# Performance work log

Hardware: AMD Instinct MI355X
Metric: run time of the kernel (lower is better)

## Reference

```python
import jax, jax.numpy as jnp
import numpy as np

N_HEADS = 16
PROJ_DIM = 64  # per-head dim
DIM = N_HEADS * PROJ_DIM  # 1024


def setup_inputs() -> dict:
    key = jax.random.key(0)
    k1, k2, k3, k4, k5 = jax.random.split(key, 5)
    N, L = 2, 2048
    scale = 1.0 / np.sqrt(DIM)
    return {
        "query": jax.random.normal(k1, (N, L, DIM), dtype=jnp.float32),
        "key": jax.random.normal(k2, (N, L, DIM), dtype=jnp.float32),
        "Wq": jax.random.normal(k3, (DIM, DIM), dtype=jnp.float32) * scale,
        "Wk": jax.random.normal(k4, (DIM, DIM), dtype=jnp.float32) * scale,
        "Wv": jax.random.normal(k5, (DIM, DIM), dtype=jnp.float32) * scale,
    }


def reference(query, key, Wq, Wk, Wv):
    # Causal linear-complexity attention (mask=True branch, left_first=False).
    N, Lq, _ = query.shape
    Lk = key.shape[1]
    H, Dh = N_HEADS, PROJ_DIM
    # torch Linear: x @ W.T ; reshape to (N, H, L, Dh)
    q = (query @ Wq.T).reshape(N, Lq, H, Dh).transpose(0, 2, 1, 3)
    k = (key @ Wk.T).reshape(N, Lk, H, Dh).transpose(0, 2, 1, 3)
    v = (key @ Wv.T).reshape(N, Lk, H, Dh).transpose(0, 2, 1, 3)
    q = jax.nn.softmax(q, axis=-1)
    k = jax.nn.softmax(k, axis=-1)
    # right[t] = sum_{s<=t} k_s^T v_s  : (N,H,Lk,Dh,Dh) cumulative outer products
    S = jnp.cumsum(jnp.einsum('nhti,nhtj->nhtij', k, v), axis=2)
    out = jnp.einsum('nhti,nhtij->nhtj', q, S)  # (N,H,Lq,Dh)
    return out.transpose(0, 2, 1, 3).reshape(N, Lq, H * Dh)
```

## Files before the change

kernel.cpp:

```cpp
#include <hip/hip_runtime.h>


constexpr int DIM  = 1024;
constexpr int H    = 16;
constexpr int DH   = 64;
constexpr int LSEQ = 2048;
constexpr int NB   = 2;
constexpr int MTOK = NB * LSEQ;
constexpr int CS   = 64;
constexpr int NC   = LSEQ / CS;

typedef __bf16 bf16x8 __attribute__((ext_vector_type(8)));
typedef float floatx4 __attribute__((ext_vector_type(4)));
typedef unsigned short ushort_t;

__device__ __forceinline__ ushort_t f2bf(float f) {
  unsigned int u = __float_as_uint(f);
  u += 0x7FFFu + ((u >> 16) & 1u);
  return (ushort_t)(u >> 16);
}
__device__ __forceinline__ float bf2f(ushort_t b) {
  return __uint_as_float(((unsigned int)b) << 16);
}

__device__ __forceinline__ void async16(void* lds, const void* g) {
  __builtin_amdgcn_global_load_lds(
      (const __attribute__((address_space(1))) unsigned int*)g,
      (__attribute__((address_space(3))) unsigned int*)lds, 16, 0, 0);
}

__device__ __forceinline__ bf16x8 tfrag(const unsigned int* T, int row, int uoff) {
  union { bf16x8 v; unsigned int u[4]; } r;
  const unsigned int* p = T + row * 33 + uoff;
  r.u[0] = p[0]; r.u[1] = p[1]; r.u[2] = p[2]; r.u[3] = p[3];
  return r.v;
}

__device__ __forceinline__ void transpose_tile(const ushort_t* g, unsigned int* TT, int tid) {
  const int ic = tid & 7, tp = tid >> 3;
  const ushort_t* r0 = g + (size_t)(2 * tp) * DIM + ic * 8;
  union { uint4 q; ushort_t u[8]; } a0, a1;
  a0.q = *(const uint4*)r0;
  a1.q = *(const uint4*)(r0 + DIM);
#pragma unroll
  for (int j = 0; j < 8; j++)
    TT[(8 * ic + j) * 33 + tp] = (unsigned int)a0.u[j] | ((unsigned int)a1.u[j] << 16);
}

__global__ __launch_bounds__(256) void cast_all(const float* __restrict__ q,
                                                const float* __restrict__ k,
                                                const float* __restrict__ wq,
                                                const float* __restrict__ wk,
                                                const float* __restrict__ wv,
                                                ushort_t* __restrict__ xbf,
                                                ushort_t* __restrict__ wbf) {
  const int seg = blockIdx.y;
  const float* src;
  ushort_t* dst;
  int n4;
  if (seg == 0)      { src = q;  dst = xbf;                  n4 = (4 << 20) / 4; }
  else if (seg == 1) { src = k;  dst = xbf + (4 << 20);      n4 = (4 << 20) / 4; }
  else if (seg == 2) { src = wq; dst = wbf;                  n4 = (1 << 20) / 4; }
  else if (seg == 3) { src = wk; dst = wbf + (1 << 20);      n4 = (1 << 20) / 4; }
  else               { src = wv; dst = wbf + (2 << 20);      n4 = (1 << 20) / 4; }
  for (int i = blockIdx.x * 256 + threadIdx.x; i < n4; i += gridDim.x * 256) {
    const float4 f = ((const float4*)src)[i];
    ((ushort4*)dst)[i] = make_ushort4(f2bf(f.x), f2bf(f.y), f2bf(f.z), f2bf(f.w));
  }
}

struct Stage { ushort_t As[128 * 32]; ushort_t Ws[128 * 32]; };
union SMemU { Stage st; ushort_t CsB[128 * 136]; };

__global__ __launch_bounds__(256) void gemm_fused(const ushort_t* __restrict__ xbf,
                                                  const ushort_t* __restrict__ wbf,
                                                  ushort_t* __restrict__ qp,
                                                  ushort_t* __restrict__ kp,
                                                  ushort_t* __restrict__ vp) {
  __shared__ SMemU sm;
  const int tid  = threadIdx.x;
  const int z    = blockIdx.z;
  const ushort_t* A = xbf + (z ? (size_t)(4 << 20) : 0);
  const ushort_t* W = wbf + (size_t)z * (1 << 20);
  ushort_t* C = (z == 0) ? qp : ((z == 1) ? kp : vp);
  const int bn   = blockIdx.x * 128;
  const int bm   = blockIdx.y * 128;
  const int lane = tid & 63;
  const int wid  = tid >> 6;
  const int wm   = wid >> 1, wn = wid & 1;
  const int row16 = lane & 15, quad = lane >> 4;

  floatx4 acc[4][4] = {};

  const ushort_t* gA0 = A + (size_t)(bm + (tid >> 2)) * DIM + (tid & 3) * 8;
  const ushort_t* gA1 = A + (size_t)(bm + 64 + (tid >> 2)) * DIM + (tid & 3) * 8;
  const ushort_t* gW0 = W + (size_t)(bn + (tid >> 2)) * DIM + (tid & 3) * 8;
  const ushort_t* gW1 = W + (size_t)(bn + 64 + (tid >> 2)) * DIM + (tid & 3) * 8;
  ushort_t* lA0 = sm.st.As + tid * 8;
  ushort_t* lA1 = sm.st.As + (tid + 256) * 8;
  ushort_t* lW0 = sm.st.Ws + tid * 8;
  ushort_t* lW1 = sm.st.Ws + (tid + 256) * 8;

  for (int k0 = 0; k0 < DIM; k0 += 32) {
    __syncthreads();
    async16(lA0, gA0 + k0);
    async16(lA1, gA1 + k0);
    async16(lW0, gW0 + k0);
    async16(lW1, gW1 + k0);
    __syncthreads();
    bf16x8 a[4], b[4];
#pragma unroll
    for (int mt = 0; mt < 4; mt++)
      a[mt] = *(const bf16x8*)&sm.st.As[(wm * 64 + mt * 16 + row16) * 32 + quad * 8];
#pragma unroll
    for (int nt = 0; nt < 4; nt++)
      b[nt] = *(const bf16x8*)&sm.st.Ws[(wn * 64 + nt * 16 + row16) * 32 + quad * 8];
#pragma unroll
    for (int mt = 0; mt < 4; mt++)
#pragma unroll
      for (int nt = 0; nt < 4; nt++)
        acc[mt][nt] = __builtin_amdgcn_mfma_f32_16x16x32_bf16(a[mt], b[nt], acc[mt][nt], 0, 0, 0);
  }
  __syncthreads();

  if (z < 2) {
#pragma unroll
    for (int mt = 0; mt < 4; mt++)
#pragma unroll
      for (int r = 0; r < 4; r++) {
        float m = fmaxf(fmaxf(acc[mt][0][r], acc[mt][1][r]),
                        fmaxf(acc[mt][2][r], acc[mt][3][r]));
#pragma unroll
        for (int o = 1; o < 16; o <<= 1) m = fmaxf(m, __shfl_xor(m, o, 64));
        float e[4], s = 0.f;
#pragma unroll
        for (int nt = 0; nt < 4; nt++) { e[nt] = __expf(acc[mt][nt][r] - m); s += e[nt]; }
#pragma unroll
        for (int o = 1; o < 16; o <<= 1) s += __shfl_xor(s, o, 64);
        const float inv = 1.f / s;
#pragma unroll
        for (int nt = 0; nt < 4; nt++) acc[mt][nt][r] = e[nt] * inv;
      }
  }

#pragma unroll
  for (int mt = 0; mt < 4; mt++)
#pragma unroll
    for (int nt = 0; nt < 4; nt++)
#pragma unroll
      for (int r = 0; r < 4; r++)
        sm.CsB[(wm * 64 + mt * 16 + quad * 4 + r) * 136 + wn * 64 + nt * 16 + row16] =
            f2bf(acc[mt][nt][r]);
  __syncthreads();
#pragma unroll
  for (int it = 0; it < 8; it++) {
    const int ch = tid + it * 256;
    const int row = ch >> 4, ic = ch & 15;
    const uint4 val = *(const uint4*)&sm.CsB[row * 136 + ic * 8];
    *(uint4*)&C[(size_t)(bm + row) * DIM + bn + ic * 8] = val;
  }
}

__global__ __launch_bounds__(256) void chunk_T(const ushort_t* __restrict__ kp,
                                               const ushort_t* __restrict__ vp,
                                               float* __restrict__ cs) {
  __shared__ unsigned int KT[64 * 33];
  __shared__ unsigned int VT[64 * 33];
  const int c = blockIdx.x, h = blockIdx.y, n = blockIdx.z;
  const int tid = threadIdx.x;
  const size_t gbase = ((size_t)(n * LSEQ + c * CS)) * DIM + h * DH;

  transpose_tile(kp + gbase, KT, tid);
  transpose_tile(vp + gbase, VT, tid);
  __syncthreads();

  const int lane = tid & 63, wid = tid >> 6;
  const int row16 = lane & 15, quad = lane >> 4;

  floatx4 acc[4] = {};
#pragma unroll
  for (int ks = 0; ks < 2; ks++) {
    const bf16x8 a = tfrag(VT, wid * 16 + row16, ks * 16 + quad * 4);
#pragma unroll
    for (int nt = 0; nt < 4; nt++) {
      const bf16x8 b = tfrag(KT, nt * 16 + row16, ks * 16 + quad * 4);
      acc[nt] = __builtin_amdgcn_mfma_f32_16x16x32_bf16(a, b, acc[nt], 0, 0, 0);
    }
  }
  float* outp = cs + ((size_t)((n * H + h) * NC + c)) * (DH * DH);
#pragma unroll
  for (int nt = 0; nt < 4; nt++)
#pragma unroll
    for (int r = 0; r < 4; r++)
      outp[(wid * 16 + quad * 4 + r) * DH + nt * 16 + row16] = acc[nt][r];
}

__global__ __launch_bounds__(256) void prefix_chunks(const float* __restrict__ cs,
                                                     ushort_t* __restrict__ csb) {
  const int nh = blockIdx.x >> 4;
  const int e  = (blockIdx.x & 15) * 256 + threadIdx.x;
  const float* bf_ = cs + (size_t)nh * NC * (DH * DH) + e;
  ushort_t* bb = csb + (size_t)nh * NC * (DH * DH) + e;
  float run = 0.f;
#pragma unroll
  for (int c = 0; c < NC; c++) {
    const float cur = bf_[(size_t)c * (DH * DH)];
    bb[(size_t)c * (DH * DH)] = f2bf(run);
    run += cur;
  }
}

__global__ __launch_bounds__(256) void attn_mfma(const ushort_t* __restrict__ qp,
                                                 const ushort_t* __restrict__ kp,
                                                 const ushort_t* __restrict__ vp,
                                                 const ushort_t* __restrict__ csb,
                                                 float* __restrict__ out) {
  __shared__ ushort_t Qs[64 * 72];
  __shared__ ushort_t Ks[64 * 72];
  __shared__ ushort_t Ts[64 * 72];
  __shared__ unsigned int VT[64 * 33];
  __shared__ ushort_t Pb[64 * 72];
  const int c = blockIdx.x, h = blockIdx.y, n = blockIdx.z;
  const int tid = threadIdx.x;
  const size_t gbase = ((size_t)(n * LSEQ + c * CS)) * DIM + h * DH;
  const size_t cbase = ((size_t)((n * H + h) * NC + c)) * (DH * DH);

#pragma unroll
  for (int it = 0; it < 2; it++) {
    const int ch = tid + it * 256;
    const int row = ch >> 3, ic = ch & 7;
    *(uint4*)&Qs[row * 72 + ic * 8] = *(const uint4*)&qp[gbase + (size_t)row * DIM + ic * 8];
    *(uint4*)&Ks[row * 72 + ic * 8] = *(const uint4*)&kp[gbase + (size_t)row * DIM + ic * 8];
    *(uint4*)&Ts[row * 72 + ic * 8] = *(const uint4*)&csb[cbase + (size_t)row * DH + ic * 8];
  }
  transpose_tile(vp + gbase, VT, tid);
  __syncthreads();

  const int lane = tid & 63, wid = tid >> 6;
  const int row16 = lane & 15, quad = lane >> 4;
  const int t0 = wid * 16;

  floatx4 acc[4] = {};
  floatx4 pacc[4] = {};

#pragma unroll
  for (int ks = 0; ks < 2; ks++) {
    const bf16x8 aq = *(const bf16x8*)&Qs[(t0 + row16) * 72 + ks * 32 + quad * 8];
#pragma unroll
    for (int nt = 0; nt < 4; nt++) {
      const bf16x8 bt = *(const bf16x8*)&Ts[(nt * 16 + row16) * 72 + ks * 32 + quad * 8];
      acc[nt] = __builtin_amdgcn_mfma_f32_16x16x32_bf16(aq, bt, acc[nt], 0, 0, 0);
      const bf16x8 bk = *(const bf16x8*)&Ks[(nt * 16 + row16) * 72 + ks * 32 + quad * 8];
      pacc[nt] = __builtin_amdgcn_mfma_f32_16x16x32_bf16(aq, bk, pacc[nt], 0, 0, 0);
    }
  }
#pragma unroll
  for (int nt = 0; nt < 4; nt++)
#pragma unroll
    for (int r = 0; r < 4; r++) {
      const int t = t0 + quad * 4 + r, s = nt * 16 + row16;
      Pb[t * 72 + s] = f2bf((s <= t) ? pacc[nt][r] : 0.f);
    }
  __syncthreads();

#pragma unroll
  for (int ks = 0; ks < 2; ks++) {
    const bf16x8 ap = *(const bf16x8*)&Pb[(t0 + row16) * 72 + ks * 32 + quad * 8];
#pragma unroll
    for (int nt = 0; nt < 4; nt++) {
      const bf16x8 bv = tfrag(VT, nt * 16 + row16, ks * 16 + quad * 4);
      acc[nt] = __builtin_amdgcn_mfma_f32_16x16x32_bf16(ap, bv, acc[nt], 0, 0, 0);
    }
  }

#pragma unroll
  for (int nt = 0; nt < 4; nt++)
#pragma unroll
    for (int r = 0; r < 4; r++)
      out[gbase + (size_t)(t0 + quad * 4 + r) * DIM + nt * 16 + row16] = acc[nt][r];
}

extern "C" void kernel_launch(void* const* d_in, const int* in_sizes, int n_in,
                              void* d_out, int out_size, void* d_ws, size_t ws_size,
                              hipStream_t stream) {
  const float* query = (const float*)d_in[0];
  const float* key   = (const float*)d_in[1];
  const float* Wq    = (const float*)d_in[2];
  const float* Wk    = (const float*)d_in[3];
  const float* Wv    = (const float*)d_in[4];
  float* out = (float*)d_out;

  const size_t PM = (size_t)4 << 20;
  ushort_t* qp = (ushort_t*)d_ws;
  ushort_t* kp = qp + PM;
  ushort_t* vp = kp + PM;
  float*    cs = (float*)(vp + PM);
  ushort_t* csb = (ushort_t*)(cs + PM);
  ushort_t* xbf = (ushort_t*)cs;
  ushort_t* wbf = (ushort_t*)out;

  cast_all<<<dim3(512, 5), 256, 0, stream>>>(query, key, Wq, Wk, Wv, xbf, wbf);

  gemm_fused<<<dim3(DIM / 128, MTOK / 128, 3), 256, 0, stream>>>(xbf, wbf, qp, kp, vp);

  chunk_T<<<dim3(NC, H, NB), 256, 0, stream>>>(kp, vp, cs);
  prefix_chunks<<<dim3(NB * H * 16), 256, 0, stream>>>(cs, csb);
  attn_mfma<<<dim3(NC, H, NB), 256, 0, stream>>>(qp, kp, vp, csb, out);
}
```

Measured before the change: 172.7 us.

## Double-buffer LDS stages in projection GEMM to overlap loads with MFMA

Splits the shared-memory staging buffer into two stages and prefetches the next K-slice of activations and weights into the alternate stage while MFMAs run on the current one. This removes one barrier per K iteration and aims to hide global-to-LDS latency behind compute. LDS footprint stays within the existing union size, but correctness depends on the async copy being complete by the barrier.

After: 161.5 us. 1.07x faster.

```diff
diff --git a/kernel.cpp b/kernel.cpp
--- a/kernel.cpp
+++ b/kernel.cpp
@@ -70,7 +70,7 @@
 }
 
 struct Stage { ushort_t As[128 * 32]; ushort_t Ws[128 * 32]; };
-union SMemU { Stage st; ushort_t CsB[128 * 136]; };
+union SMemU { Stage st[2]; ushort_t CsB[128 * 136]; };
 
 __global__ __launch_bounds__(256) void gemm_fused(const ushort_t* __restrict__ xbf,
                                                   const ushort_t* __restrict__ wbf,
@@ -96,32 +96,41 @@
   const ushort_t* gA1 = A + (size_t)(bm + 64 + (tid >> 2)) * DIM + (tid & 3) * 8;
   const ushort_t* gW0 = W + (size_t)(bn + (tid >> 2)) * DIM + (tid & 3) * 8;
   const ushort_t* gW1 = W + (size_t)(bn + 64 + (tid >> 2)) * DIM + (tid & 3) * 8;
-  ushort_t* lA0 = sm.st.As + tid * 8;
-  ushort_t* lA1 = sm.st.As + (tid + 256) * 8;
-  ushort_t* lW0 = sm.st.Ws + tid * 8;
-  ushort_t* lW1 = sm.st.Ws + (tid + 256) * 8;
-
+
+  {
+    Stage& s0 = sm.st[0];
+    async16(s0.As + tid * 8,         gA0);
+    async16(s0.As + (tid + 256) * 8, gA1);
+    async16(s0.Ws + tid * 8,         gW0);
+    async16(s0.Ws + (tid + 256) * 8, gW1);
+  }
+  __syncthreads();
+
+  int cur = 0;
   for (int k0 = 0; k0 < DIM; k0 += 32) {
-    __syncthreads();
-    async16(lA0, gA0 + k0);
-    async16(lA1, gA1 + k0);
-    async16(lW0, gW0 + k0);
-    async16(lW1, gW1 + k0);
-    __syncthreads();
+    if (k0 + 32 < DIM) {
+      Stage& sn = sm.st[cur ^ 1];
+      async16(sn.As + tid * 8,         gA0 + k0 + 32);
+      async16(sn.As + (tid + 256) * 8, gA1 + k0 + 32);
+      async16(sn.Ws + tid * 8,         gW0 + k0 + 32);
+      async16(sn.Ws + (tid + 256) * 8, gW1 + k0 + 32);
+    }
+    const Stage& s = sm.st[cur];
     bf16x8 a[4], b[4];
 #pragma unroll
     for (int mt = 0; mt < 4; mt++)
-      a[mt] = *(const bf16x8*)&sm.st.As[(wm * 64 + mt * 16 + row16) * 32 + quad * 8];
+      a[mt] = *(const bf16x8*)&s.As[(wm * 64 + mt * 16 + row16) * 32 + quad * 8];
 #pragma unroll
     for (int nt = 0; nt < 4; nt++)
-      b[nt] = *(const bf16x8*)&sm.st.Ws[(wn * 64 + nt * 16 + row16) * 32 + quad * 8];
+      b[nt] = *(const bf16x8*)&s.Ws[(wn * 64 + nt * 16 + row16) * 32 + quad * 8];
 #pragma unroll
     for (int mt = 0; mt < 4; mt++)
 #pragma unroll
       for (int nt = 0; nt < 4; nt++)
         acc[mt][nt] = __builtin_amdgcn_mfma_f32_16x16x32_bf16(a[mt], b[nt], acc[mt][nt], 0, 0, 0);
-  }
-  __syncthreads();
+    __syncthreads();
+    cur ^= 1;
+  }
 
   if (z < 2) {
 #pragma unroll
```

## Triple-buffer GEMM LDS stages with async prefetch and XOR-swizzled layout

Applied to the files above, without the earlier changes.

Replaces the single-buffer load-sync-compute loop in the projection GEMM with a three-stage ring of LDS buffers. Global-to-LDS async copies are issued two k-steps ahead and gated by vmcnt waits, so memory latency can overlap the MFMA work. Column groups are XOR-swizzled on both the write and read side to reduce LDS bank conflicts on the fragment reads. LDS use per block rises to about 48KB, which may lower occupancy.

Result: faster. 158.2 us (-8.4%).

```diff
diff --git a/kernel.cpp b/kernel.cpp
--- a/kernel.cpp
+++ b/kernel.cpp
@@ -70,7 +70,7 @@
 }
 
 struct Stage { ushort_t As[128 * 32]; ushort_t Ws[128 * 32]; };
-union SMemU { Stage st; ushort_t CsB[128 * 136]; };
+union SMemU { Stage st[3]; ushort_t CsB[128 * 136]; };
 
 __global__ __launch_bounds__(256) void gemm_fused(const ushort_t* __restrict__ xbf,
                                                   const ushort_t* __restrict__ wbf,
@@ -92,35 +92,54 @@
 
   floatx4 acc[4][4] = {};
 
-  const ushort_t* gA0 = A + (size_t)(bm + (tid >> 2)) * DIM + (tid & 3) * 8;
-  const ushort_t* gA1 = A + (size_t)(bm + 64 + (tid >> 2)) * DIM + (tid & 3) * 8;
-  const ushort_t* gW0 = W + (size_t)(bn + (tid >> 2)) * DIM + (tid & 3) * 8;
-  const ushort_t* gW1 = W + (size_t)(bn + 64 + (tid >> 2)) * DIM + (tid & 3) * 8;
-  ushort_t* lA0 = sm.st.As + tid * 8;
-  ushort_t* lA1 = sm.st.As + (tid + 256) * 8;
-  ushort_t* lW0 = sm.st.Ws + tid * 8;
-  ushort_t* lW1 = sm.st.Ws + (tid + 256) * 8;
-
-  for (int k0 = 0; k0 < DIM; k0 += 32) {
-    __syncthreads();
-    async16(lA0, gA0 + k0);
-    async16(lA1, gA1 + k0);
-    async16(lW0, gW0 + k0);
-    async16(lW1, gW1 + k0);
-    __syncthreads();
+  const int srow = tid >> 2;
+  const int cg   = (tid & 3) ^ ((srow ^ (srow >> 2)) & 3);
+  const ushort_t* gA0 = A + (size_t)(bm + srow) * DIM + cg * 8;
+  const ushort_t* gA1 = A + (size_t)(bm + 64 + srow) * DIM + cg * 8;
+  const ushort_t* gW0 = W + (size_t)(bn + srow) * DIM + cg * 8;
+  const ushort_t* gW1 = W + (size_t)(bn + 64 + srow) * DIM + cg * 8;
+
+#define STAGE(buf, koff)                                    \
+  {                                                         \
+    Stage& s_ = sm.st[buf];                                 \
+    async16(s_.As + tid * 8,         gA0 + (koff));         \
+    async16(s_.As + (tid + 256) * 8, gA1 + (koff));         \
+    async16(s_.Ws + tid * 8,         gW0 + (koff));         \
+    async16(s_.Ws + (tid + 256) * 8, gW1 + (koff));         \
+  }
+
+  const int qx   = quad ^ ((row16 ^ (row16 >> 2)) & 3);
+  const int aoff = (wm * 64 + row16) * 32 + qx * 8;
+  const int boff = (wn * 64 + row16) * 32 + qx * 8;
+
+  STAGE(0, 0);
+  STAGE(1, 32);
+
+  int cur = 0, pf = 2;
+  for (int s = 0; s < 32; ++s) {
+    if (s < 31) asm volatile("s_waitcnt vmcnt(4)" ::: "memory");
+    else        asm volatile("s_waitcnt vmcnt(0)" ::: "memory");
+    __builtin_amdgcn_s_barrier();
+    if (s + 2 < 32) STAGE(pf, (s + 2) * 32);
+
+    const Stage& st = sm.st[cur];
     bf16x8 a[4], b[4];
 #pragma unroll
     for (int mt = 0; mt < 4; mt++)
-      a[mt] = *(const bf16x8*)&sm.st.As[(wm * 64 + mt * 16 + row16) * 32 + quad * 8];
+      a[mt] = *(const bf16x8*)&st.As[aoff + mt * 512];
 #pragma unroll
     for (int nt = 0; nt < 4; nt++)
-      b[nt] = *(const bf16x8*)&sm.st.Ws[(wn * 64 + nt * 16 + row16) * 32 + quad * 8];
+      b[nt] = *(const bf16x8*)&st.Ws[boff + nt * 512];
 #pragma unroll
     for (int mt = 0; mt < 4; mt++)
 #pragma unroll
       for (int nt = 0; nt < 4; nt++)
         acc[mt][nt] = __builtin_amdgcn_mfma_f32_16x16x32_bf16(a[mt], b[nt], acc[mt][nt], 0, 0, 0);
-  }
+
+    cur = (cur == 2) ? 0 : cur + 1;
+    pf  = (pf  == 2) ? 0 : pf + 1;
+  }
+#undef STAGE
   __syncthreads();
 
   if (z < 2) {
```

## Restructure projection GEMM with 256x256 tiles, double-buffered LDS, swizzle and XCD mapping

Applied to the files above, without the earlier changes.

The QKV projection GEMM moves from 128x128 tiles on 256 threads to 256x256 tiles on 512 threads, with each wave computing 128x64. Global-to-LDS loads are double-buffered with explicit vmcnt waits so the next K-slice loads while MFMAs run, and LDS columns are XOR-swizzled to cut bank conflicts. Blocks are remapped so consecutive tiles land on the same XCD for L2 reuse, and the epilogue writes out in four 64-row passes to fit the smaller staging buffer. Only 192 blocks launch, so occupancy is lower, and the larger accumulator array raises register pressure.

After: 156.3 us. -9.5%, faster.

```diff
diff --git a/kernel.cpp b/kernel.cpp
--- a/kernel.cpp
+++ b/kernel.cpp
@@ -18,9 +18,6 @@
   unsigned int u = __float_as_uint(f);
   u += 0x7FFFu + ((u >> 16) & 1u);
   return (ushort_t)(u >> 16);
-}
-__device__ __forceinline__ float bf2f(ushort_t b) {
-  return __uint_as_float(((unsigned int)b) << 16);
 }
 
 __device__ __forceinline__ void async16(void* lds, const void* g) {
@@ -69,63 +66,108 @@
   }
 }
 
-struct Stage { ushort_t As[128 * 32]; ushort_t Ws[128 * 32]; };
-union SMemU { Stage st; ushort_t CsB[128 * 136]; };
-
-__global__ __launch_bounds__(256) void gemm_fused(const ushort_t* __restrict__ xbf,
-                                                  const ushort_t* __restrict__ wbf,
-                                                  ushort_t* __restrict__ qp,
-                                                  ushort_t* __restrict__ kp,
-                                                  ushort_t* __restrict__ vp) {
+struct Stage2 { ushort_t As[256 * 32]; ushort_t Ws[256 * 32]; };
+union SMemU { Stage2 st[2]; ushort_t CsB[64 * 264]; };
+
+__global__ __launch_bounds__(512, 2) void gemm_fused(const ushort_t* __restrict__ xbf,
+                                                     const ushort_t* __restrict__ wbf,
+                                                     ushort_t* __restrict__ qp,
+                                                     ushort_t* __restrict__ kp,
+                                                     ushort_t* __restrict__ vp) {
   __shared__ SMemU sm;
-  const int tid  = threadIdx.x;
-  const int z    = blockIdx.z;
+  const int tid = threadIdx.x;
+
+  const int xcd   = blockIdx.x & 7;
+  const int local = blockIdx.x >> 3;
+  const int T     = xcd * 24 + local;
+  const int z     = T >> 6;
+  const int rem   = T & 63;
+  const int bm    = (rem >> 2) * 256;
+  const int bn    = (rem & 3) * 256;
+
   const ushort_t* A = xbf + (z ? (size_t)(4 << 20) : 0);
   const ushort_t* W = wbf + (size_t)z * (1 << 20);
   ushort_t* C = (z == 0) ? qp : ((z == 1) ? kp : vp);
-  const int bn   = blockIdx.x * 128;
-  const int bm   = blockIdx.y * 128;
-  const int lane = tid & 63;
-  const int wid  = tid >> 6;
-  const int wm   = wid >> 1, wn = wid & 1;
+
+  const int lane  = tid & 63;
+  const int wid   = tid >> 6;
+  const int wr    = wid >> 2, wc = wid & 3;
   const int row16 = lane & 15, quad = lane >> 4;
 
-  floatx4 acc[4][4] = {};
-
-  const ushort_t* gA0 = A + (size_t)(bm + (tid >> 2)) * DIM + (tid & 3) * 8;
-  const ushort_t* gA1 = A + (size_t)(bm + 64 + (tid >> 2)) * DIM + (tid & 3) * 8;
-  const ushort_t* gW0 = W + (size_t)(bn + (tid >> 2)) * DIM + (tid & 3) * 8;
-  const ushort_t* gW1 = W + (size_t)(bn + 64 + (tid >> 2)) * DIM + (tid & 3) * 8;
-  ushort_t* lA0 = sm.st.As + tid * 8;
-  ushort_t* lA1 = sm.st.As + (tid + 256) * 8;
-  ushort_t* lW0 = sm.st.Ws + tid * 8;
-  ushort_t* lW1 = sm.st.Ws + (tid + 256) * 8;
-
-  for (int k0 = 0; k0 < DIM; k0 += 32) {
-    __syncthreads();
-    async16(lA0, gA0 + k0);
-    async16(lA1, gA1 + k0);
-    async16(lW0, gW0 + k0);
-    async16(lW1, gW1 + k0);
-    __syncthreads();
-    bf16x8 a[4], b[4];
-#pragma unroll
-    for (int mt = 0; mt < 4; mt++)
-      a[mt] = *(const bf16x8*)&sm.st.As[(wm * 64 + mt * 16 + row16) * 32 + quad * 8];
-#pragma unroll
-    for (int nt = 0; nt < 4; nt++)
-      b[nt] = *(const bf16x8*)&sm.st.Ws[(wn * 64 + nt * 16 + row16) * 32 + quad * 8];
-#pragma unroll
-    for (int mt = 0; mt < 4; mt++)
-#pragma unroll
-      for (int nt = 0; nt < 4; nt++)
-        acc[mt][nt] = __builtin_amdgcn_mfma_f32_16x16x32_bf16(a[mt], b[nt], acc[mt][nt], 0, 0, 0);
-  }
-  __syncthreads();
+  floatx4 acc[8][4] = {};
+
+  const int srow = tid >> 2;
+  const int lc   = (tid & 3) ^ ((srow ^ (srow >> 2)) & 3);
+  const ushort_t* pA0 = A + (size_t)(bm + srow) * DIM + lc * 8;
+  const ushort_t* pA1 = A + (size_t)(bm + 128 + srow) * DIM + lc * 8;
+  const ushort_t* pW0 = W + (size_t)(bn + srow) * DIM + lc * 8;
+  const ushort_t* pW1 = W + (size_t)(bn + 128 + srow) * DIM + lc * 8;
+
+#define STAGEB(B, kt)                                         \
+  {                                                           \
+    ushort_t* As_ = sm.st[B].As;                              \
+    ushort_t* Ws_ = sm.st[B].Ws;                              \
+    const int ko = (kt) * 32;                                 \
+    async16(As_ + tid * 8,         pA0 + ko);                 \
+    async16(As_ + (tid + 512) * 8, pA1 + ko);                 \
+    async16(Ws_ + tid * 8,         pW0 + ko);                 \
+    async16(Ws_ + (tid + 512) * 8, pW1 + ko);                 \
+  }
+
+  const int xq    = quad ^ ((row16 ^ (row16 >> 2)) & 3);
+  const int aBase = (wr * 128 + row16) * 32 + xq * 8;
+  const int bBase = (wc * 64 + row16) * 32 + xq * 8;
+
+  bf16x8 aF0[8], bF0[4], aF1[8], bF1[4];
+
+#define READB(B, AF, BF)                                                      \
+  {                                                                           \
+    _Pragma("unroll")                                                         \
+    for (int mt = 0; mt < 8; mt++)                                            \
+      AF[mt] = *(const bf16x8*)&sm.st[B].As[aBase + mt * 512];                \
+    _Pragma("unroll")                                                         \
+    for (int nt = 0; nt < 4; nt++)                                            \
+      BF[nt] = *(const bf16x8*)&sm.st[B].Ws[bBase + nt * 512];                \
+  }
+
+#define MFMAB(AF, BF)                                                         \
+  {                                                                           \
+    _Pragma("unroll")                                                         \
+    for (int mt = 0; mt < 8; mt++)                                            \
+      _Pragma("unroll")                                                       \
+      for (int nt = 0; nt < 4; nt++)                                          \
+        acc[mt][nt] = __builtin_amdgcn_mfma_f32_16x16x32_bf16(                \
+            AF[mt], BF[nt], acc[mt][nt], 0, 0, 0);                            \
+  }
+
+  STAGEB(0, 0);
+  STAGEB(1, 1);
+  asm volatile("s_waitcnt vmcnt(4)" ::: "memory");
+  __builtin_amdgcn_s_barrier();
+  READB(0, aF0, bF0);
+
+#pragma unroll
+  for (int kt = 0; kt < 32; ++kt) {
+    asm volatile("s_waitcnt lgkmcnt(0)" ::: "memory");
+    __builtin_amdgcn_s_barrier();
+    if (kt + 2 < 32) {
+      if ((kt & 1) == 0) { STAGEB(0, kt + 2); } else { STAGEB(1, kt + 2); }
+    }
+    if (kt + 1 < 32) {
+      if (kt + 2 < 32) { asm volatile("s_waitcnt vmcnt(4)" ::: "memory"); }
+      else             { asm volatile("s_waitcnt vmcnt(0)" ::: "memory"); }
+      __builtin_amdgcn_s_barrier();
+      if ((kt & 1) == 0) { READB(1, aF1, bF1); } else { READB(0, aF0, bF0); }
+    }
+    if ((kt & 1) == 0) { MFMAB(aF0, bF0); } else { MFMAB(aF1, bF1); }
+  }
+#undef STAGEB
+#undef READB
+#undef MFMAB
 
   if (z < 2) {
 #pragma unroll
-    for (int mt = 0; mt < 4; mt++)
+    for (int mt = 0; mt < 8; mt++)
 #pragma unroll
       for (int r = 0; r < 4; r++) {
         float m = fmaxf(fmaxf(acc[mt][0][r], acc[mt][1][r]),
@@ -144,20 +186,27 @@
   }
 
 #pragma unroll
-  for (int mt = 0; mt < 4; mt++)
-#pragma unroll
-    for (int nt = 0; nt < 4; nt++)
-#pragma unroll
-      for (int r = 0; r < 4; r++)
-        sm.CsB[(wm * 64 + mt * 16 + quad * 4 + r) * 136 + wn * 64 + nt * 16 + row16] =
-            f2bf(acc[mt][nt][r]);
-  __syncthreads();
-#pragma unroll
-  for (int it = 0; it < 8; it++) {
-    const int ch = tid + it * 256;
-    const int row = ch >> 4, ic = ch & 15;
-    const uint4 val = *(const uint4*)&sm.CsB[row * 136 + ic * 8];
-    *(uint4*)&C[(size_t)(bm + row) * DIM + bn + ic * 8] = val;
+  for (int p = 0; p < 4; ++p) {
+    __syncthreads();
+    if (wr == (p >> 1)) {
+      const int mh = (p & 1) * 4;
+#pragma unroll
+      for (int m4 = 0; m4 < 4; m4++)
+#pragma unroll
+        for (int nt = 0; nt < 4; nt++)
+#pragma unroll
+          for (int r = 0; r < 4; r++)
+            sm.CsB[(m4 * 16 + quad * 4 + r) * 264 + wc * 64 + nt * 16 + row16] =
+                f2bf(acc[mh + m4][nt][r]);
+    }
+    __syncthreads();
+#pragma unroll
+    for (int it = 0; it < 4; it++) {
+      const int ch = tid + it * 512;
+      const int row = ch >> 5, ic = ch & 31;
+      *(uint4*)&C[(size_t)(bm + p * 64 + row) * DIM + bn + ic * 8] =
+          *(const uint4*)&sm.CsB[row * 264 + ic * 8];
+    }
   }
 }
 
@@ -301,7 +350,7 @@
 
   cast_all<<<dim3(512, 5), 256, 0, stream>>>(query, key, Wq, Wk, Wv, xbf, wbf);
 
-  gemm_fused<<<dim3(DIM / 128, MTOK / 128, 3), 256, 0, stream>>>(xbf, wbf, qp, kp, vp);
+  gemm_fused<<<dim3(192), 512, 0, stream>>>(xbf, wbf, qp, kp, vp);
 
   chunk_T<<<dim3(NC, H, NB), 256, 0, stream>>>(kp, vp, cs);
   prefix_chunks<<<dim3(NB * H * 16), 256, 0, stream>>>(cs, csb);
```
